# Kernel tuning notes

Measured on AMD Instinct MI355X. Metric: run time of the kernel, lower is better.

## Reference

```python
import jax, jax.numpy as jnp
import numpy as np

B, H, W, DIM = 32, 32, 40, 224
HEADS, DH, WS = 8, 28, 8
INNER = HEADS * DH                      # 224 == DIM (required by spectral branch view)
D_MODEL, D_STATE, D_CONV = 32, 16, 4    # mamba: d_model = H since mode='b h w c'
D_INNER, DT_RANK = 64, 2                # expand=2 -> 64; ceil(32/16)=2
RS = 0.7071067811865476                 # 1/sqrt(2), Haar (db1) filter coefficient


def _ln(x, g, b):
    m = x.mean(-1, keepdims=True)
    v = ((x - m) ** 2).mean(-1, keepdims=True)
    return (x - m) * jax.lax.rsqrt(v + 1e-5) * g + b


def _l2n(x):
    return x / jnp.maximum(jnp.linalg.norm(x, axis=-1, keepdims=True), 1e-12)


def _dwt2(x):
    # Haar level-1 2D DWT, pywt ordering (cA,(cH,cV,cD)); x: [b,c,H,W], even H,W
    lo = (x[..., 0::2] + x[..., 1::2]) * RS
    hi = (x[..., 0::2] - x[..., 1::2]) * RS
    cA = (lo[..., 0::2, :] + lo[..., 1::2, :]) * RS
    cH = (lo[..., 0::2, :] - lo[..., 1::2, :]) * RS
    cV = (hi[..., 0::2, :] + hi[..., 1::2, :]) * RS
    cD = (hi[..., 0::2, :] - hi[..., 1::2, :]) * RS
    return cA, cH, cV, cD


def _iwt2(cA, cH, cV, cD):
    b, c, hh, ww = cA.shape
    lo = jnp.stack([(cA + cH) * RS, (cA - cH) * RS], -2).reshape(b, c, 2 * hh, ww)
    hi = jnp.stack([(cV + cD) * RS, (cV - cD) * RS], -2).reshape(b, c, 2 * hh, ww)
    return jnp.stack([(lo + hi) * RS, (lo - hi) * RS], -1).reshape(b, c, 2 * hh, 2 * ww)


def _mamba(xf, in_proj_W, conv1d_W, conv1d_b, x_proj_W, dt_proj_W, dt_proj_b,
           A_log, Dp, out_proj_W):
    # xf: [b, L, D_MODEL]; mamba_ssm selective-scan math
    bsz = xf.shape[0]
    xz = xf @ in_proj_W                                   # [b,L,2*D_INNER]
    xi, z = xz[..., :D_INNER], xz[..., D_INNER:]
    xc = jax.lax.conv_general_dilated(
        xi.transpose(0, 2, 1), conv1d_W[:, None, :], (1,), [(D_CONV - 1, 0)],
        dimension_numbers=('NCH', 'OIH', 'NCH'), feature_group_count=D_INNER)
    xc = jax.nn.silu(xc + conv1d_b[None, :, None]).transpose(0, 2, 1)  # [b,L,D_INNER]
    x_dbl = xc @ x_proj_W
    dt = jax.nn.softplus(x_dbl[..., :DT_RANK] @ dt_proj_W + dt_proj_b)  # [b,L,D_INNER]
    Bm = x_dbl[..., DT_RANK:DT_RANK + D_STATE]
    Cm = x_dbl[..., DT_RANK + D_STATE:]
    A = -jnp.exp(A_log)                                   # [D_INNER, D_STATE]

    def step(hst, inp):
        dt_t, B_t, C_t, u_t = inp
        dA = jnp.exp(dt_t[:, :, None] * A)                # [b,d,n]
        hst = dA * hst + (dt_t * u_t)[:, :, None] * B_t[:, None, :]
        return hst, jnp.einsum('bdn,bn->bd', hst, C_t)

    h0 = jnp.zeros((bsz, D_INNER, D_STATE), xf.dtype)
    xs = tuple(jnp.moveaxis(t, 1, 0) for t in (dt, Bm, Cm, xc))
    _, ys = jax.lax.scan(step, h0, xs)
    y = jnp.moveaxis(ys, 0, 1) + xc * Dp
    y = y * jax.nn.silu(z)
    return y @ out_proj_W


def setup_inputs():
    key = jax.random.key(0)
    ks = iter(jax.random.split(key, 48))
    def rnd(shape, s=0.02):
        return jax.random.normal(next(ks), shape, jnp.float32) * s
    inp = {}
    inp['x'] = jax.random.normal(next(ks), (B, H, W, DIM), jnp.float32)
    inp['Wq'] = rnd((DIM, INNER)); inp['Wkv'] = rnd((DIM, 2 * INNER))
    inp['ln_g'] = jnp.ones((D_MODEL,)); inp['ln_b'] = jnp.zeros((D_MODEL,))
    inp['in_proj_W'] = rnd((D_MODEL, 2 * D_INNER))
    inp['conv1d_W'] = rnd((D_INNER, D_CONV), 0.3); inp['conv1d_b'] = jnp.zeros((D_INNER,))
    inp['x_proj_W'] = rnd((D_INNER, DT_RANK + 2 * D_STATE), 0.1)
    inp['dt_proj_W'] = rnd((DT_RANK, D_INNER), 0.5)
    inp['dt_proj_b'] = jnp.full((D_INNER,), -4.6, jnp.float32)
    inp['A_log'] = jnp.tile(jnp.log(jnp.arange(1, D_STATE + 1, dtype=jnp.float32))[None], (D_INNER, 1))
    inp['Dp'] = jnp.ones((D_INNER,))
    inp['out_proj_W'] = rnd((D_INNER, D_MODEL))
    inp['skip_scale'] = jnp.ones((1,))
    inp['proj_W'] = rnd((D_MODEL, D_MODEL)); inp['proj_b'] = jnp.zeros((D_MODEL,))
    inp['conv3d_W'] = rnd((1, 1, 5, 5, 5), 0.05); inp['conv3d_b'] = jnp.zeros((1,))
    inp['Wq1'] = rnd((DIM, INNER)); inp['Wkv1'] = rnd((DIM, 2 * INNER))
    inp['pos_emb'] = jnp.clip(rnd((1, HEADS, WS * WS, WS * WS), 1.0), -2.0, 2.0)
    for i in (1, 2, 3, 4):
        inp['Wo%d' % i] = rnd((INNER, DIM)); inp['bo%d' % i] = jnp.zeros((DIM,))
    return inp


def reference(x, Wq, Wkv, ln_g, ln_b, in_proj_W, conv1d_W, conv1d_b, x_proj_W,
              dt_proj_W, dt_proj_b, A_log, Dp, out_proj_W, skip_scale, proj_W,
              proj_b, conv3d_W, conv3d_b, Wq1, Wkv1, pos_emb,
              Wo1, bo1, Wo2, bo2, Wo3, bo3, Wo4, bo4):
    b, h, w, c = x.shape
    scale = DH ** -0.5
    N = h * w
    # ---- spectral branch: channel-wise cosine-similarity attention ----
    x_in = x.reshape(b, N, c)
    q = (x_in @ Wq).reshape(b, N, HEADS, DH).transpose(0, 2, 3, 1)   # [b,Hd,dh,N]
    kv = x_in @ Wkv
    k = kv[..., :INNER].reshape(b, N, HEADS, DH).transpose(0, 2, 3, 1)
    v = kv[..., INNER:].reshape(b, N, HEADS, DH).transpose(0, 2, 3, 1)
    attn = jax.nn.softmax(jnp.einsum('bhin,bhjn->bhij', _l2n(k), _l2n(q)) * scale, -1)
    xa = jnp.einsum('bhij,bhjn->bhin', attn, v)                      # [b,Hd,dh,N]
    x = xa.transpose(0, 3, 1, 2).reshape(b, h, w, c) + x
    # ---- MambaLayer (mode 'b h w c': channel axis = h) + residual ----
    xf = x.reshape(b, h, w * c).transpose(0, 2, 1)                   # [b, w*c, h]
    xn = _ln(xf, ln_g, ln_b)
    xm = _mamba(xn, in_proj_W, conv1d_W, conv1d_b, x_proj_W, dt_proj_W,
                dt_proj_b, A_log, Dp, out_proj_W) + skip_scale * xn
    xm = _ln(xm, ln_g, ln_b) @ proj_W + proj_b
    x = xm.transpose(0, 2, 1).reshape(b, h, w, c) + x
    # ---- Conv3d 5x5x5 fusion over (h,w,c) ----
    x = jax.lax.conv_general_dilated(x[:, None], conv3d_W, (1, 1, 1), [(2, 2)] * 3,
            dimension_numbers=('NCDHW', 'OIDHW', 'NCDHW'))[:, 0] + conv3d_b[0]
    # ---- local branch: Haar subbands + windowed attention with pos bias ----
    cA, cH, cV, cD = _dwt2(x.transpose(0, 3, 1, 2))
    ha, wa = cA.shape[2], cA.shape[3]
    pad_h, pad_w = (-ha) % WS, (-wa) % WS

    def win_attn(sub, Wo, bo):
        s = jnp.pad(sub, ((0, 0), (0, 0), (0, pad_h), (0, pad_w)), mode='reflect')
        Hs, Ws_ = s.shape[2], s.shape[3]
        xw = s.reshape(b, c, Hs // WS, WS, Ws_ // WS, WS).transpose(0, 2, 4, 3, 5, 1)
        xw = xw.reshape(-1, WS * WS, c)
        qw = (xw @ Wq1).reshape(-1, WS * WS, HEADS, DH).transpose(0, 2, 1, 3) * scale
        kvw = xw @ Wkv1
        kw = kvw[..., :INNER].reshape(-1, WS * WS, HEADS, DH).transpose(0, 2, 1, 3)
        vw = kvw[..., INNER:].reshape(-1, WS * WS, HEADS, DH).transpose(0, 2, 1, 3)
        a = jax.nn.softmax(jnp.einsum('bhid,bhjd->bhij', qw, kw) + pos_emb, -1)
        o = jnp.einsum('bhij,bhjd->bhid', a, vw).transpose(0, 2, 1, 3).reshape(-1, WS * WS, INNER)
        o = (o @ Wo + bo).reshape(b, Hs // WS, Ws_ // WS, WS, WS, c).transpose(0, 1, 3, 2, 4, 5)
        return o.reshape(b, Hs, Ws_, c)[:, :ha, :wa, :].transpose(0, 3, 1, 2)

    out = _iwt2(win_attn(cA, Wo1, bo1), win_attn(cH, Wo2, bo2),
                win_attn(cV, Wo3, bo3), win_attn(cD, Wo4, bo4))
    return out.transpose(0, 2, 3, 1)
```

## Files before the change

kernel.cpp:

```cpp
#include <hip/hip_runtime.h>
#include <hip/hip_bf16.h>
#include <math.h>

typedef __hip_bfloat16 bf16;
typedef __attribute__((ext_vector_type(8))) short bf16x8;
typedef __attribute__((ext_vector_type(4))) float f32x4;

__device__ __forceinline__ float b2f(bf16 v){ return __bfloat162float(v); }
__device__ __forceinline__ bf16  f2b(float v){ return __float2bfloat16(v); }
__device__ __forceinline__ float bfbits(unsigned u){ return __uint_as_float(u << 16); }
__device__ __forceinline__ unsigned short b2us(bf16 v){ union { bf16 b; unsigned short u; } c; c.b = v; return c.u; }
__device__ __forceinline__ void unpack8(uint4 q, float* f){
  f[0]=bfbits(q.x&0xffffu); f[1]=bfbits(q.x>>16);
  f[2]=bfbits(q.y&0xffffu); f[3]=bfbits(q.y>>16);
  f[4]=bfbits(q.z&0xffffu); f[5]=bfbits(q.z>>16);
  f[6]=bfbits(q.w&0xffffu); f[7]=bfbits(q.w>>16);
}
__device__ __forceinline__ uint4 pack8f(const float* f){
  uint4 q;
  q.x = (unsigned)b2us(f2b(f[0])) | ((unsigned)b2us(f2b(f[1]))<<16);
  q.y = (unsigned)b2us(f2b(f[2])) | ((unsigned)b2us(f2b(f[3]))<<16);
  q.z = (unsigned)b2us(f2b(f[4])) | ((unsigned)b2us(f2b(f[5]))<<16);
  q.w = (unsigned)b2us(f2b(f[6])) | ((unsigned)b2us(f2b(f[7]))<<16);
  return q;
}

#define NTOK 1280
#define LSEQ 8960
#define CHLEN 140
#define ATT_SCALE 0.1889822365046136f
#define LOG2E 1.4426950408889634f

__global__ __launch_bounds__(256) void cvt_bf16_kernel(const float* __restrict__ src, bf16* __restrict__ dst, int n8) {
  int i = blockIdx.x*256 + threadIdx.x;
  if (i >= n8) return;
  const float4* s = (const float4*)(src + (size_t)i*8);
  float4 a = s[0], b = s[1];
  float f[8] = {a.x,a.y,a.z,a.w,b.x,b.y,b.z,b.w};
  *(uint4*)(dst + (size_t)i*8) = pack8f(f);
}

__global__ __launch_bounds__(256) void transpose_bf16_kernel(const float* __restrict__ W, bf16* __restrict__ Wt,
                                                             int K, int N) {
  int idx = blockIdx.x*256 + threadIdx.x;
  if (idx >= N*K) return;
  int n = idx / K, k = idx % K;
  Wt[idx] = f2b(W[(size_t)k*N + n]);
}

__global__ __launch_bounds__(256) void mfma_gemm_kernel(const bf16* __restrict__ A, const bf16* __restrict__ Bt,
                                                        float* __restrict__ C, int M, int N, int K) {
  __shared__ short As[64][40];
  __shared__ short Bs[64][40];
  const int tid = threadIdx.x;
  const int wave = tid >> 6, lane = tid & 63;
  const int m0 = blockIdx.y*64, n0 = blockIdx.x*64;
  const int lrow = tid >> 2, lseg = (tid & 3) * 8;
  const int mrow = wave*16 + (lane & 15);
  const int kq = (lane >> 4) * 8;
  f32x4 acc[4] = {};
  for (int k0 = 0; k0 < K; k0 += 32) {
    uint4 av = *(const uint4*)(A + (size_t)(m0+lrow)*K + k0 + lseg);
    uint4 bv = make_uint4(0u,0u,0u,0u);
    if (n0 + lrow < N) bv = *(const uint4*)(Bt + (size_t)(n0+lrow)*K + k0 + lseg);
    __syncthreads();
    *(uint4*)&As[lrow][lseg] = av;
    *(uint4*)&Bs[lrow][lseg] = bv;
    __syncthreads();
    bf16x8 af = *(const bf16x8*)&As[mrow][kq];
#pragma unroll
    for (int nt = 0; nt < 4; ++nt) {
      bf16x8 bfv = *(const bf16x8*)&Bs[nt*16 + (lane & 15)][kq];
      acc[nt] = __builtin_amdgcn_mfma_f32_16x16x32_bf16(af, bfv, acc[nt], 0, 0, 0);
    }
  }
  const int quad = lane >> 4, col = lane & 15;
#pragma unroll
  for (int nt = 0; nt < 4; ++nt) {
    int n = n0 + nt*16 + col;
    if (n >= N) continue;
#pragma unroll
    for (int r = 0; r < 4; ++r) {
      int m = m0 + wave*16 + quad*4 + r;
      C[(size_t)m*N + n] = acc[nt][r];
    }
  }
}

__global__ __launch_bounds__(256) void zero_kernel(float* __restrict__ p, int n) {
  int i = blockIdx.x*256 + threadIdx.x;
  if (i < n) p[i] = 0.f;
}

__global__ __launch_bounds__(256) void colnorm_kernel(const float* __restrict__ qb, const float* __restrict__ kvb,
                                                      float* __restrict__ nqs, float* __restrict__ nks) {
  const int b  = blockIdx.x >> 4;
  const int nc = blockIdx.x & 15;
  const int tid = threadIdx.x;
  __shared__ float lq[224], lk[224];
  if (tid < 224) { lq[tid] = 0.f; lk[tid] = 0.f; }
  __syncthreads();
  const int n0 = nc * 80;
  for (int idx = tid; idx < 80*224; idx += 256) {
    int n = n0 + idx / 224, c = idx % 224;
    float v = qb[((size_t)(b*NTOK + n))*224 + c];
    atomicAdd(&lq[c], v*v);
    float w = kvb[((size_t)(b*NTOK + n))*448 + c];
    atomicAdd(&lk[c], w*w);
  }
  __syncthreads();
  if (tid < 224) {
    atomicAdd(&nqs[b*224 + tid], lq[tid]);
    atomicAdd(&nks[b*224 + tid], lk[tid]);
  }
}

__global__ __launch_bounds__(256) void gram_kernel(const float* __restrict__ qb, const float* __restrict__ kvb,
                                                   const float* __restrict__ nqs, const float* __restrict__ nks,
                                                   float* __restrict__ attnA) {
  const int b = blockIdx.x >> 3, hd = blockIdx.x & 7;
  const int tid = threadIdx.x;
  __shared__ float kt[32][28];
  __shared__ float qt[32][28];
  __shared__ float sc[784];
  float acc[4] = {0.f,0.f,0.f,0.f};
  for (int nt = 0; nt < NTOK; nt += 32) {
    __syncthreads();
    for (int idx = tid; idx < 896; idx += 256) {
      int r = idx / 28, c = idx % 28;
      kt[r][c] = kvb[((size_t)(b*NTOK + nt + r))*448 + hd*28 + c];
      qt[r][c] = qb [((size_t)(b*NTOK + nt + r))*224 + hd*28 + c];
    }
    __syncthreads();
#pragma unroll
    for (int p = 0; p < 4; ++p) {
      int idx = tid + p*256;
      if (idx < 784) {
        int i = idx / 28, j = idx % 28;
        float s = 0.f;
#pragma unroll
        for (int r = 0; r < 32; ++r) s = fmaf(kt[r][i], qt[r][j], s);
        acc[p] += s;
      }
    }
  }
  __syncthreads();
#pragma unroll
  for (int p = 0; p < 4; ++p) {
    int idx = tid + p*256;
    if (idx < 784) {
      int i = idx / 28, j = idx % 28;
      float nk = fmaxf(sqrtf(nks[b*224 + hd*28 + i]), 1e-12f);
      float nq = fmaxf(sqrtf(nqs[b*224 + hd*28 + j]), 1e-12f);
      sc[idx] = acc[p] * ATT_SCALE / (nk * nq);
    }
  }
  __syncthreads();
  if (tid < 28) {
    int i = tid;
    float mx = -1e30f;
#pragma unroll
    for (int j = 0; j < 28; ++j) mx = fmaxf(mx, sc[i*28+j]);
    float e[28]; float s = 0.f;
#pragma unroll
    for (int j = 0; j < 28; ++j) { e[j] = expf(sc[i*28+j] - mx); s += e[j]; }
    float inv = 1.f / s;
#pragma unroll
    for (int j = 0; j < 28; ++j) attnA[(size_t)blockIdx.x*784 + i*28 + j] = e[j]*inv;
  }
}

__global__ __launch_bounds__(256) void applyattn_kernel(const float* __restrict__ attnA, const float* __restrict__ kvb,
                                                        const float* __restrict__ x, float* __restrict__ x1) {
  const int bhd = blockIdx.x;
  const int b = bhd >> 3, hd = bhd & 7;
  const int tid = threadIdx.x;
  __shared__ float a[784];
  for (int idx = tid; idx < 784; idx += 256) a[idx] = attnA[(size_t)bhd*784 + idx];
  __syncthreads();
  const int i = tid % 28;
  const int n = blockIdx.y * 9 + tid / 28;
  if (tid < 252 && n < NTOK) {
    const float* vrow = &kvb[((size_t)(b*NTOK + n))*448 + 224 + hd*28];
    float s = 0.f;
#pragma unroll
    for (int j = 0; j < 28; ++j) s = fmaf(a[i*28+j], vrow[j], s);
    size_t o = ((size_t)(b*NTOK + n))*224 + hd*28 + i;
    x1[o] = s + x[o];
  }
}

__global__ __launch_bounds__(256) void mamba_in_kernel(const float* __restrict__ x1, const float* __restrict__ lng,
                                                       const float* __restrict__ lnb, const float* __restrict__ Wip,
                                                       bf16* __restrict__ xi) {
  __shared__ float W[2048];
  __shared__ float g[32], bb[32];
  const int tid = threadIdx.x;
  const int b = blockIdx.y;
  const int t = blockIdx.x*256 + tid;
  for (int idx = tid; idx < 2048; idx += 256) {
    int d = idx >> 5, m = idx & 31;
    W[idx] = Wip[m*128 + d];
  }
  if (tid < 32) { g[tid] = lng[tid]; bb[tid] = lnb[tid]; }
  __syncthreads();
  float xv[32];
  float mean = 0.f;
#pragma unroll
  for (int m = 0; m < 32; ++m) { xv[m] = x1[((size_t)(b*32+m))*LSEQ + t]; mean += xv[m]; }
  mean *= (1.f/32.f);
  float var = 0.f;
#pragma unroll
  for (int m = 0; m < 32; ++m) { float d = xv[m]-mean; var = fmaf(d, d, var); }
  var *= (1.f/32.f);
  const float rstd = rsqrtf(var + 1e-5f);
  float xn[32];
#pragma unroll
  for (int m = 0; m < 32; ++m) xn[m] = (xv[m]-mean)*rstd*g[m] + bb[m];
  bf16* row = xi + ((size_t)b*LSEQ + t)*64;
#pragma unroll
  for (int gi = 0; gi < 8; ++gi) {
    float sv[8];
#pragma unroll
    for (int j = 0; j < 8; ++j) {
      int d = gi*8 + j;
      float s = 0.f;
#pragma unroll
      for (int mq = 0; mq < 8; ++mq) {
        float4 w = *(const float4*)&W[d*32 + mq*4];
        s = fmaf(xn[mq*4+0], w.x, s);
        s = fmaf(xn[mq*4+1], w.y, s);
        s = fmaf(xn[mq*4+2], w.z, s);
        s = fmaf(xn[mq*4+3], w.w, s);
      }
      sv[j] = s;
    }
    *(uint4*)(row + gi*8) = pack8f(sv);
  }
}

__global__ __launch_bounds__(256) void mamba_conv_kernel(const bf16* __restrict__ xi, const float* __restrict__ convW,
    const float* __restrict__ convB, const float* __restrict__ xpW, const float* __restrict__ dtW,
    const float* __restrict__ dtB, bf16* __restrict__ xc, bf16* __restrict__ dts,
    bf16* __restrict__ Bc, bf16* __restrict__ Ccs) {
  __shared__ float xit[67][65];
  __shared__ float xct[64][65];
  __shared__ float xdbl[64][36];
  __shared__ float Wc[256], bcs[64], Wxp[2176], Wdt[128], bdt[64];
  const int tid = threadIdx.x;
  const int b = blockIdx.y;
  const int t0 = blockIdx.x * 64;

  if (tid < 256) Wc[tid] = convW[tid];
  for (int idx = tid; idx < 2176; idx += 256) Wxp[idx] = xpW[idx];
  if (tid < 128) Wdt[tid] = dtW[tid];
  if (tid < 64) { bcs[tid] = convB[tid]; bdt[tid] = dtB[tid]; }
  for (int idx = tid; idx < 67*8; idx += 256) {
    const int row = idx >> 3, seg = idx & 7;
    const int gt = t0 + row - 3;
    float f[8];
    if (gt >= 0) {
      uint4 q = *(const uint4*)(xi + ((size_t)b*LSEQ + gt)*64 + seg*8);
      unpack8(q, f);
    } else {
#pragma unroll
      for (int j = 0; j < 8; ++j) f[j] = 0.f;
    }
#pragma unroll
    for (int j = 0; j < 8; ++j) xit[row][seg*8 + j] = f[j];
  }
  __syncthreads();

  {
    const int tl = tid >> 2, cg = tid & 3;
    float sv[16];
#pragma unroll
    for (int j = 0; j < 16; ++j) {
      const int d = cg*16 + j;
      float s = bcs[d];
      s = fmaf(xit[tl+0][d], Wc[d*4+0], s);
      s = fmaf(xit[tl+1][d], Wc[d*4+1], s);
      s = fmaf(xit[tl+2][d], Wc[d*4+2], s);
      s = fmaf(xit[tl+3][d], Wc[d*4+3], s);
      s = s / (1.f + expf(-s));
      xct[tl][d] = s;
      sv[j] = s;
    }
    bf16* out = xc + ((size_t)b*LSEQ + t0 + tl)*64 + cg*16;
    *(uint4*)(out)     = pack8f(sv);
    *(uint4*)(out + 8) = pack8f(sv + 8);
  }
  __syncthreads();

  {
    const int tl = tid & 63, g = tid >> 6;
    for (int n = g; n < 34; n += 4) {
      float s = 0.f;
#pragma unroll
      for (int d = 0; d < 64; ++d) s = fmaf(xct[tl][d], Wxp[d*34 + n], s);
      xdbl[tl][n] = s;
    }
  }
  __syncthreads();

  if (tid < 256) {
    const int which = tid >> 7;
    const int idx = tid & 127;
    const int tl = idx >> 1, half = idx & 1;
    const float* src = &xdbl[tl][2 + which*16 + half*8];
    bf16* dst = (which ? Ccs : Bc) + ((size_t)b*LSEQ + t0 + tl)*16 + half*8;
    *(uint4*)dst = pack8f(src);
  }
  {
    const int tl = tid >> 2, cg = tid & 3;
    const float x0 = xdbl[tl][0], x1v = xdbl[tl][1];
    float sv[16];
#pragma unroll
    for (int j = 0; j < 16; ++j) {
      const int d = cg*16 + j;
      float v = fmaf(x0, Wdt[d], fmaf(x1v, Wdt[64+d], bdt[d]));
      v = (v > 20.f) ? v : log1pf(expf(v));
      sv[j] = v;
    }
    bf16* out = dts + ((size_t)b*LSEQ + t0 + tl)*64 + cg*16;
    *(uint4*)(out)     = pack8f(sv);
    *(uint4*)(out + 8) = pack8f(sv + 8);
  }
}

__global__ __launch_bounds__(256) void scan1_kernel(const bf16* __restrict__ dts, const bf16* __restrict__ xc,
    const bf16* __restrict__ Bc, const float* __restrict__ Alog, float* __restrict__ P, float* __restrict__ F) {
  const int b = blockIdx.x >> 6, chk = blockIdx.x & 63;
  const int tid = threadIdx.x;
  const int d = tid >> 2, ng = tid & 3;
  float A2[4], Pr[4], Fr[4];
#pragma unroll
  for (int j = 0; j < 4; ++j) {
    A2[j] = -expf(Alog[d*16 + ng*4 + j]) * LOG2E;
    Pr[j] = 1.f; Fr[j] = 0.f;
  }
  const size_t tbase = (size_t)b*LSEQ + (size_t)chk*CHLEN;
  for (int i = 0; i < CHLEN; ++i) {
    const size_t t = tbase + i;
    float dtv = b2f(dts[t*64 + d]);
    float u   = b2f(xc [t*64 + d]);
    float du  = dtv*u;
    uint2 bq = *(const uint2*)(Bc + t*16 + ng*4);
    float Bv[4];
    Bv[0]=bfbits(bq.x&0xffffu); Bv[1]=bfbits(bq.x>>16);
    Bv[2]=bfbits(bq.y&0xffffu); Bv[3]=bfbits(bq.y>>16);
#pragma unroll
    for (int j = 0; j < 4; ++j) {
      float a = exp2f(dtv*A2[j]);
      Pr[j] *= a;
      Fr[j] = fmaf(a, Fr[j], du*Bv[j]);
    }
  }
  const size_t o = (((size_t)(b*64 + chk))*64 + d)*16 + ng*4;
  *(float4*)(P + o) = make_float4(Pr[0],Pr[1],Pr[2],Pr[3]);
  *(float4*)(F + o) = make_float4(Fr[0],Fr[1],Fr[2],Fr[3]);
}

__global__ __launch_bounds__(256) void scan2_kernel(const float* __restrict__ P, const float* __restrict__ F,
                                                    float* __restrict__ H0) {
  const int idx = blockIdx.x*256 + threadIdx.x;
  const int b = idx >> 10, dn = idx & 1023;
  const size_t base = (size_t)b*64*1024 + dn;
  float h = 0.f;
  for (int ch = 0; ch < 64; ++ch) {
    const size_t a = base + (size_t)ch*1024;
    H0[a] = h;
    h = fmaf(P[a], h, F[a]);
  }
}

__global__ __launch_bounds__(256) void scan3_kernel(const bf16* __restrict__ dts, const bf16* __restrict__ xc,
    const bf16* __restrict__ Bc, const bf16* __restrict__ Ccs, const float* __restrict__ Alog,
    const float* __restrict__ Dp, const float* __restrict__ H0, bf16* __restrict__ y) {
  const int b = blockIdx.x >> 6, chk = blockIdx.x & 63;
  const int tid = threadIdx.x;
  const int d = tid >> 2, ng = tid & 3;
  float A2[4], h[4];
  const size_t hb = (((size_t)(b*64 + chk))*64 + d)*16 + ng*4;
  float4 h0 = *(const float4*)(H0 + hb);
  h[0]=h0.x; h[1]=h0.y; h[2]=h0.z; h[3]=h0.w;
#pragma unroll
  for (int j = 0; j < 4; ++j) A2[j] = -expf(Alog[d*16 + ng*4 + j]) * LOG2E;
  const float Dpd = Dp[d];
  const size_t tbase = (size_t)b*LSEQ + (size_t)chk*CHLEN;
  for (int i = 0; i < CHLEN; ++i) {
    const size_t t = tbase + i;
    float dtv = b2f(dts[t*64 + d]);
    float u   = b2f(xc [t*64 + d]);
    float du  = dtv*u;
    uint2 bq = *(const uint2*)(Bc  + t*16 + ng*4);
    uint2 cq = *(const uint2*)(Ccs + t*16 + ng*4);
    float Bv[4], Cv[4];
    Bv[0]=bfbits(bq.x&0xffffu); Bv[1]=bfbits(bq.x>>16);
    Bv[2]=bfbits(bq.y&0xffffu); Bv[3]=bfbits(bq.y>>16);
    Cv[0]=bfbits(cq.x&0xffffu); Cv[1]=bfbits(cq.x>>16);
    Cv[2]=bfbits(cq.y&0xffffu); Cv[3]=bfbits(cq.y>>16);
    float p = 0.f;
#pragma unroll
    for (int j = 0; j < 4; ++j) {
      float a = exp2f(dtv*A2[j]);
      h[j] = fmaf(a, h[j], du*Bv[j]);
      p = fmaf(h[j], Cv[j], p);
    }
    p += __shfl_xor(p, 1);
    p += __shfl_xor(p, 2);
    if (ng == 0) y[t*64 + d] = f2b(p + u*Dpd);
  }
}

__global__ __launch_bounds__(256) void mamba_out_kernel(float* __restrict__ x1, const bf16* __restrict__ y,
    const float* __restrict__ lng, const float* __restrict__ lnb, const float* __restrict__ Wip,
    const float* __restrict__ Wout, const float* __restrict__ skipp, const float* __restrict__ Wp,
    const float* __restrict__ pbias) {
  __shared__ float Wzt[2048];
  __shared__ float Wo[2048];
  __shared__ float Pwt[1024];
  __shared__ float g[32], bb[32], pb[32];
  __shared__ float sskip;
  const int tid = threadIdx.x;
  for (int idx = tid; idx < 2048; idx += 256) {
    int d = idx >> 5, m = idx & 31;
    Wzt[idx] = Wip[m*128 + 64 + d];
  }
  for (int idx = tid; idx < 2048; idx += 256) Wo[idx] = Wout[idx];
  for (int idx = tid; idx < 1024; idx += 256) {
    int m2 = idx >> 5, m = idx & 31;
    Pwt[idx] = Wp[m*32 + m2];
  }
  if (tid < 32) { g[tid] = lng[tid]; bb[tid] = lnb[tid]; pb[tid] = pbias[tid]; }
  if (tid == 0) sskip = skipp[0];
  __syncthreads();
  const int b = blockIdx.y;
  const int t = blockIdx.x*256 + tid;
  float xv[32];
  float mean = 0.f;
#pragma unroll
  for (int m = 0; m < 32; ++m) { xv[m] = x1[((size_t)(b*32+m))*LSEQ + t]; mean += xv[m]; }
  mean *= (1.f/32.f);
  float var = 0.f;
#pragma unroll
  for (int m = 0; m < 32; ++m) { float d = xv[m]-mean; var = fmaf(d, d, var); }
  var *= (1.f/32.f);
  const float rstd = rsqrtf(var + 1e-5f);
  float xn[32];
#pragma unroll
  for (int m = 0; m < 32; ++m) xn[m] = (xv[m]-mean)*rstd*g[m] + bb[m];
  float out[32] = {};
  const bf16* yrow = y + ((size_t)b*LSEQ + t)*64;
#pragma unroll
  for (int gi = 0; gi < 8; ++gi) {
    uint4 q = *(const uint4*)(yrow + gi*8);
    float yv8[8]; unpack8(q, yv8);
#pragma unroll
    for (int j = 0; j < 8; ++j) {
      int d = gi*8 + j;
      float zd = 0.f;
#pragma unroll
      for (int mq = 0; mq < 8; ++mq) {
        float4 w = *(const float4*)&Wzt[d*32 + mq*4];
        zd = fmaf(xn[mq*4+0], w.x, zd);
        zd = fmaf(xn[mq*4+1], w.y, zd);
        zd = fmaf(xn[mq*4+2], w.z, zd);
        zd = fmaf(xn[mq*4+3], w.w, zd);
      }
      float gd = yv8[j] * zd / (1.f + expf(-zd));
#pragma unroll
      for (int mq = 0; mq < 8; ++mq) {
        float4 w = *(const float4*)&Wo[d*32 + mq*4];
        out[mq*4+0] = fmaf(gd, w.x, out[mq*4+0]);
        out[mq*4+1] = fmaf(gd, w.y, out[mq*4+1]);
        out[mq*4+2] = fmaf(gd, w.z, out[mq*4+2]);
        out[mq*4+3] = fmaf(gd, w.w, out[mq*4+3]);
      }
    }
  }
#pragma unroll
  for (int m = 0; m < 32; ++m) out[m] = fmaf(sskip, xn[m], out[m]);
  float mean2 = 0.f;
#pragma unroll
  for (int m = 0; m < 32; ++m) mean2 += out[m];
  mean2 *= (1.f/32.f);
  float var2 = 0.f;
#pragma unroll
  for (int m = 0; m < 32; ++m) { float d = out[m]-mean2; var2 = fmaf(d, d, var2); }
  var2 *= (1.f/32.f);
  const float rstd2 = rsqrtf(var2 + 1e-5f);
#pragma unroll
  for (int m = 0; m < 32; ++m) out[m] = (out[m]-mean2)*rstd2*g[m] + bb[m];
  for (int m2 = 0; m2 < 32; ++m2) {
    float r = pb[m2];
#pragma unroll
    for (int mq = 0; mq < 8; ++mq) {
      float4 w = *(const float4*)&Pwt[m2*32 + mq*4];
      r = fmaf(out[mq*4+0], w.x, r);
      r = fmaf(out[mq*4+1], w.y, r);
      r = fmaf(out[mq*4+2], w.z, r);
      r = fmaf(out[mq*4+3], w.w, r);
    }
    x1[((size_t)(b*32+m2))*LSEQ + t] = r + xv[m2];
  }
}

__global__ __launch_bounds__(256) void conv3d_kernel(const float* __restrict__ x2, const float* __restrict__ w,
                                                     const float* __restrict__ bias, float* __restrict__ x3) {
  __shared__ float ww[125];
  __shared__ float b0;
  const int tid = threadIdx.x;
  if (tid < 125) ww[tid] = w[tid];
  if (tid == 0) b0 = bias[0];
  __syncthreads();
  const int gid = blockIdx.x*256 + tid;
  const int kg = gid % 28;
  int r = gid / 28;
  const int j = r % 40; r /= 40;
  const int i = r % 32; const int b = r / 32;
  const int k0 = kg * 8;
  float acc[8] = {};
  for (int di = 0; di < 5; ++di) {
    int ii = i + di - 2; if (ii < 0 || ii >= 32) continue;
    for (int dj = 0; dj < 5; ++dj) {
      int jj = j + dj - 2; if (jj < 0 || jj >= 40) continue;
      const float* row = &x2[(((size_t)(b*32+ii))*40 + jj)*224];
      float f[16];
#pragma unroll
      for (int off = 0; off < 4; ++off) {
        int base = k0 + off*4 - 4;
        if (base >= 0 && base <= 220) {
          float4 v = *(const float4*)(row + base);
          f[off*4+0]=v.x; f[off*4+1]=v.y; f[off*4+2]=v.z; f[off*4+3]=v.w;
        } else {
          f[off*4+0]=0.f; f[off*4+1]=0.f; f[off*4+2]=0.f; f[off*4+3]=0.f;
        }
      }
      const float* wr = &ww[(di*5+dj)*5];
#pragma unroll
      for (int dk = 0; dk < 5; ++dk) {
        float wv = wr[dk];
#pragma unroll
        for (int o = 0; o < 8; ++o) acc[o] = fmaf(wv, f[o+dk+2], acc[o]);
      }
    }
  }
  float* out = x3 + (size_t)gid*8;
  *(float4*)(out)     = make_float4(acc[0]+b0, acc[1]+b0, acc[2]+b0, acc[3]+b0);
  *(float4*)(out + 4) = make_float4(acc[4]+b0, acc[5]+b0, acc[6]+b0, acc[7]+b0);
}

__global__ __launch_bounds__(256) void dwtwin_kernel(const float* __restrict__ x3, bf16* __restrict__ xw) {
  const int gid = blockIdx.x*256 + threadIdx.x;
  const int ch = gid % 224; int r = gid / 224;
  const int tok = r % 64; const int win = r / 64;
  const int b = win / 6, rr = win % 6, wy = rr / 3, wx = rr % 3;
  const int ty = tok >> 3, tx = tok & 7;
  const int i = wy*8 + ty;
  const int jp = wx*8 + tx;
  const int j = (jp < 20) ? jp : (38 - jp);
  const size_t base = (((size_t)(b*32 + 2*i))*40 + 2*j)*224 + ch;
  const float v00 = x3[base];
  const float v01 = x3[base + 224];
  const float v10 = x3[base + 8960];
  const float v11 = x3[base + 8960 + 224];
  const size_t o = (size_t)r*224 + ch;
  const size_t SW = 2752512;
  xw[o]        = f2b(0.5f*(v00 + v01 + v10 + v11));
  xw[SW + o]   = f2b(0.5f*(v00 + v01 - v10 - v11));
  xw[2*SW + o] = f2b(0.5f*(v00 - v01 + v10 - v11));
  xw[3*SW + o] = f2b(0.5f*(v00 - v01 - v10 + v11));
}

__global__ __launch_bounds__(256) void winattn_kernel(const float* __restrict__ qw, const float* __restrict__ kvw,
                                                      const float* __restrict__ pos, bf16* __restrict__ ow) {
  const int win = blockIdx.x >> 3, hd = blockIdx.x & 7;
  const int tid = threadIdx.x;
  __shared__ float qs[1792], ks[1792], vs[1792];
  __shared__ float sc[4096];
  for (int idx = tid; idx < 1792; idx += 256) {
    int tok = idx / 28, d = idx % 28;
    qs[idx] = qw [((size_t)(win*64+tok))*224 + hd*28 + d] * ATT_SCALE;
    ks[idx] = kvw[((size_t)(win*64+tok))*448 + hd*28 + d];
    vs[idx] = kvw[((size_t)(win*64+tok))*448 + 224 + hd*28 + d];
  }
  __syncthreads();
#pragma unroll
  for (int p = 0; p < 16; ++p) {
    int idx = tid + p*256;
    int i = idx >> 6, j = idx & 63;
    float a = 0.f;
#pragma unroll
    for (int d = 0; d < 28; ++d) a = fmaf(qs[i*28+d], ks[j*28+d], a);
    sc[idx] = a + pos[(hd*64 + i)*64 + j];
  }
  __syncthreads();
  if (tid < 64) {
    const int i = tid;
    float mx = -1e30f;
#pragma unroll
    for (int j = 0; j < 64; ++j) mx = fmaxf(mx, sc[i*64+j]);
    float s = 0.f;
#pragma unroll
    for (int j = 0; j < 64; ++j) { float e = expf(sc[i*64+j] - mx); sc[i*64+j] = e; s += e; }
    const float inv = 1.f / s;
#pragma unroll
    for (int j = 0; j < 64; ++j) sc[i*64+j] *= inv;
  }
  __syncthreads();
  for (int idx = tid; idx < 1792; idx += 256) {
    int i = idx / 28, d = idx % 28;
    float a = 0.f;
#pragma unroll
    for (int j = 0; j < 64; ++j) a = fmaf(sc[i*64+j], vs[j*28+d], a);
    ow[((size_t)(win*64+i))*224 + hd*28 + d] = f2b(a);
  }
}

__global__ __launch_bounds__(256) void scatter_kernel(const float* __restrict__ proj, const float* __restrict__ bo,
                                                      float* __restrict__ wa) {
  const int gid = blockIdx.x*256 + threadIdx.x;
  const int ch = gid % 224; int r = gid / 224;
  const int tok = r % 64; const int win = r / 64;
  const int b = win / 6, rr = win % 6, wy = rr / 3, wx = rr % 3;
  const int ty = tok >> 3, tx = tok & 7;
  const int i = wy*8 + ty;
  const int jp = wx*8 + tx;
  if (jp < 20)
    wa[(((size_t)(b*16+i))*20 + jp)*224 + ch] = proj[gid] + bo[ch];
}

__global__ __launch_bounds__(256) void iwt_kernel(const float* __restrict__ wa, float* __restrict__ out) {
  const int gid = blockIdx.x*256 + threadIdx.x;
  const int ch = gid % 224; int r = gid / 224;
  const int j2 = r % 40; r /= 40;
  const int i2 = r % 32; const int b = r / 32;
  const size_t SB = 2293760;
  const size_t base = (((size_t)(b*16 + (i2>>1)))*20 + (j2>>1))*224 + ch;
  const float cA = wa[base];
  const float cH = wa[SB + base];
  const float cV = wa[2*SB + base];
  const float cD = wa[3*SB + base];
  const float sp = (i2 & 1) ? -1.f : 1.f;
  const float sq = (j2 & 1) ? -1.f : 1.f;
  out[gid] = 0.5f*(cA + sp*cH + sq*cV + sp*sq*cD);
}

extern "C" void kernel_launch(void* const* d_in, const int* in_sizes, int n_in,
                              void* d_out, int out_size, void* d_ws, size_t ws_size,
                              hipStream_t stream) {
  (void)in_sizes; (void)n_in; (void)out_size; (void)ws_size;
  const float* x     = (const float*)d_in[0];
  const float* Wq    = (const float*)d_in[1];
  const float* Wkv   = (const float*)d_in[2];
  const float* lng   = (const float*)d_in[3];
  const float* lnb   = (const float*)d_in[4];
  const float* Wip   = (const float*)d_in[5];
  const float* convW = (const float*)d_in[6];
  const float* convB = (const float*)d_in[7];
  const float* xpW   = (const float*)d_in[8];
  const float* dtW   = (const float*)d_in[9];
  const float* dtB   = (const float*)d_in[10];
  const float* Alog  = (const float*)d_in[11];
  const float* Dp    = (const float*)d_in[12];
  const float* Wout  = (const float*)d_in[13];
  const float* skip  = (const float*)d_in[14];
  const float* Wp    = (const float*)d_in[15];
  const float* pbias = (const float*)d_in[16];
  const float* c3w   = (const float*)d_in[17];
  const float* c3b   = (const float*)d_in[18];
  const float* Wq1   = (const float*)d_in[19];
  const float* Wkv1  = (const float*)d_in[20];
  const float* pos   = (const float*)d_in[21];

  char* ws = (char*)d_ws;
  float* x1    = (float*)(ws + 0);
  float* qbuf  = (float*)(ws + 36700160);
  float* kvbuf = (float*)(ws + 73400320);
  bf16*  WqT   = (bf16*) (ws + 146800640);
  bf16*  WkvT  = (bf16*) (ws + 146900992);
  bf16*  xbf   = (bf16*) (ws + 147101696);
  bf16*  xi    = (bf16*) (ws + 36700160);
  bf16*  xc    = (bf16*) (ws + 73400320);
  bf16*  dts   = (bf16*) (ws + 110100480);
  bf16*  Bcb   = (bf16*) (ws + 146800640);
  bf16*  Ccb   = (bf16*) (ws + 155975680);
  float* Pbuf  = (float*)(ws + 165150720);
  float* Fbuf  = (float*)(ws + 173539328);
  float* H0    = (float*)(ws + 181927936);
  bf16*  ybuf  = (bf16*) (ws + 36700160);
  float* x3    = (float*)(ws + 36700160);
  bf16*  xw    = (bf16*) (ws + 73400320);
  float* qw    = (float*)(ws + 95420416);
  float* kvw   = (float*)(ws + 106430464);
  bf16*  owb   = (bf16*) (ws + 128450560);
  bf16*  Wq1T  = (bf16*) (ws + 134000640);
  bf16*  Wkv1T = (bf16*) (ws + 134100992);
  bf16*  WoT0  = (bf16*) (ws + 134301696);
  bf16*  WoT1  = (bf16*) (ws + 134402048);
  bf16*  WoT2  = (bf16*) (ws + 134502400);
  bf16*  WoT3  = (bf16*) (ws + 134602752);
  float* projt = qw;
  float* wab   = (float*)(ws + 0);
  float* nqs   = (float*)(ws + 190316544);
  float* nks   = (float*)(ws + 190345216);
  float* attnA = (float*)(ws + 190373888);
  bf16* WoTs[4] = {WoT0, WoT1, WoT2, WoT3};

  zero_kernel<<<56, 256, 0, stream>>>(nqs, 14336);
  cvt_bf16_kernel<<<4480, 256, 0, stream>>>(x, xbf, 1146880);
  transpose_bf16_kernel<<<196, 256, 0, stream>>>(Wq,  WqT,  224, 224);
  transpose_bf16_kernel<<<392, 256, 0, stream>>>(Wkv, WkvT, 224, 448);
  mfma_gemm_kernel<<<dim3(4,640), 256, 0, stream>>>(xbf, WqT,  qbuf,  40960, 224, 224);
  mfma_gemm_kernel<<<dim3(7,640), 256, 0, stream>>>(xbf, WkvT, kvbuf, 40960, 448, 224);
  colnorm_kernel<<<512, 256, 0, stream>>>(qbuf, kvbuf, nqs, nks);
  gram_kernel<<<256, 256, 0, stream>>>(qbuf, kvbuf, nqs, nks, attnA);
  applyattn_kernel<<<dim3(256,143), 256, 0, stream>>>(attnA, kvbuf, x, x1);

  mamba_in_kernel<<<dim3(35,32), 256, 0, stream>>>(x1, lng, lnb, Wip, xi);
  mamba_conv_kernel<<<dim3(140,32), 256, 0, stream>>>(xi, convW, convB, xpW, dtW, dtB, xc, dts, Bcb, Ccb);
  scan1_kernel<<<2048, 256, 0, stream>>>(dts, xc, Bcb, Alog, Pbuf, Fbuf);
  scan2_kernel<<<128, 256, 0, stream>>>(Pbuf, Fbuf, H0);
  scan3_kernel<<<2048, 256, 0, stream>>>(dts, xc, Bcb, Ccb, Alog, Dp, H0, ybuf);
  mamba_out_kernel<<<dim3(35,32), 256, 0, stream>>>(x1, ybuf, lng, lnb, Wip, Wout, skip, Wp, pbias);

  conv3d_kernel<<<4480, 256, 0, stream>>>(x1, c3w, c3b, x3);

  dwtwin_kernel<<<10752, 256, 0, stream>>>(x3, xw);
  transpose_bf16_kernel<<<196, 256, 0, stream>>>(Wq1,  Wq1T,  224, 224);
  transpose_bf16_kernel<<<392, 256, 0, stream>>>(Wkv1, Wkv1T, 224, 448);
  for (int s = 0; s < 4; ++s)
    transpose_bf16_kernel<<<196, 256, 0, stream>>>((const float*)d_in[22 + 2*s], WoTs[s], 224, 224);
  for (int s = 0; s < 4; ++s) {
    const float* bo = (const float*)d_in[23 + 2*s];
    const bf16* xws = xw + (size_t)s * 2752512;
    mfma_gemm_kernel<<<dim3(4,192), 256, 0, stream>>>(xws, Wq1T,  qw,  12288, 224, 224);
    mfma_gemm_kernel<<<dim3(7,192), 256, 0, stream>>>(xws, Wkv1T, kvw, 12288, 448, 224);
    winattn_kernel<<<1536, 256, 0, stream>>>(qw, kvw, pos, owb);
    mfma_gemm_kernel<<<dim3(4,192), 256, 0, stream>>>(owb, WoTs[s], projt, 12288, 224, 224);
    scatter_kernel<<<10752, 256, 0, stream>>>(projt, bo, wab + (size_t)s * 2293760);
  }
  iwt_kernel<<<35840, 256, 0, stream>>>(wab, (float*)d_out);
}
```

Measured before the change: 1.694 ms.

## Keep mamba conv and x_proj in registers with shuffle reductions

The mamba_conv kernel no longer stages the input window, conv output and x_proj results in shared-memory tiles. Each thread now loads its four causal input rows straight into registers and computes its 16 conv channels there. It then produces partial x_proj dot products that are reduced across the four channel-group lanes with xor shuffles. A small new kernel pre-transposes x_proj_W so the per-output weight reads are contiguous float4 loads. This removes two block barriers and a large amount of shared memory, in exchange for more registers per thread, redundant shuffle work and an extra tiny launch whose buffer reuses the nqs workspace region.

```diff
diff --git a/kernel.cpp b/kernel.cpp
--- a/kernel.cpp
+++ b/kernel.cpp
@@ -46,6 +46,13 @@
   if (idx >= N*K) return;
   int n = idx / K, k = idx % K;
   Wt[idx] = f2b(W[(size_t)k*N + n]);
+}
+
+__global__ __launch_bounds__(256) void transpose_xp_kernel(const float* __restrict__ W, float* __restrict__ Wt) {
+  int idx = blockIdx.x*256 + threadIdx.x;
+  if (idx >= 2176) return;
+  int n = idx >> 6, d = idx & 63;
+  Wt[idx] = W[d*34 + n];
 }
 
 __global__ __launch_bounds__(256) void mfma_gemm_kernel(const bf16* __restrict__ A, const bf16* __restrict__ Bt,
@@ -240,91 +247,99 @@
 }
 
 __global__ __launch_bounds__(256) void mamba_conv_kernel(const bf16* __restrict__ xi, const float* __restrict__ convW,
-    const float* __restrict__ convB, const float* __restrict__ xpW, const float* __restrict__ dtW,
+    const float* __restrict__ convB, const float* __restrict__ xpWT, const float* __restrict__ dtW,
     const float* __restrict__ dtB, bf16* __restrict__ xc, bf16* __restrict__ dts,
     bf16* __restrict__ Bc, bf16* __restrict__ Ccs) {
-  __shared__ float xit[67][65];
-  __shared__ float xct[64][65];
-  __shared__ float xdbl[64][36];
-  __shared__ float Wc[256], bcs[64], Wxp[2176], Wdt[128], bdt[64];
+  __shared__ float Wc[256], bcs[64], Wxpt[2176], Wdt[128], bdt[64];
   const int tid = threadIdx.x;
   const int b = blockIdx.y;
   const int t0 = blockIdx.x * 64;
+  const int tl = tid >> 2, cg = tid & 3;
 
   if (tid < 256) Wc[tid] = convW[tid];
-  for (int idx = tid; idx < 2176; idx += 256) Wxp[idx] = xpW[idx];
+  for (int idx = tid; idx < 2176; idx += 256) Wxpt[idx] = xpWT[idx];
   if (tid < 128) Wdt[tid] = dtW[tid];
   if (tid < 64) { bcs[tid] = convB[tid]; bdt[tid] = dtB[tid]; }
-  for (int idx = tid; idx < 67*8; idx += 256) {
-    const int row = idx >> 3, seg = idx & 7;
-    const int gt = t0 + row - 3;
-    float f[8];
+  __syncthreads();
+
+  const int t = t0 + tl;
+  uint4 r4[4][2];
+#pragma unroll
+  for (int k = 0; k < 4; ++k) {
+    const int gt = t - 3 + k;
     if (gt >= 0) {
-      uint4 q = *(const uint4*)(xi + ((size_t)b*LSEQ + gt)*64 + seg*8);
-      unpack8(q, f);
+      const bf16* rp = xi + ((size_t)b*LSEQ + gt)*64 + cg*16;
+      r4[k][0] = *(const uint4*)(rp);
+      r4[k][1] = *(const uint4*)(rp + 8);
     } else {
-#pragma unroll
-      for (int j = 0; j < 8; ++j) f[j] = 0.f;
-    }
-#pragma unroll
-    for (int j = 0; j < 8; ++j) xit[row][seg*8 + j] = f[j];
-  }
-  __syncthreads();
-
+      r4[k][0] = make_uint4(0u,0u,0u,0u);
+      r4[k][1] = make_uint4(0u,0u,0u,0u);
+    }
+  }
+
+  float sv[16];
+#pragma unroll
+  for (int j = 0; j < 16; ++j) {
+    const int d = cg*16 + j;
+    float4 wc = *(const float4*)&Wc[d*4];
+    float s = bcs[d];
+#pragma unroll
+    for (int k = 0; k < 4; ++k) {
+      const uint4 q = r4[k][j >> 3];
+      const int w = (j >> 1) & 3;
+      unsigned comp = (w==0) ? q.x : (w==1) ? q.y : (w==2) ? q.z : q.w;
+      float xv = bfbits((j & 1) ? (comp >> 16) : (comp & 0xffffu));
+      float wk = (k==0) ? wc.x : (k==1) ? wc.y : (k==2) ? wc.z : wc.w;
+      s = fmaf(xv, wk, s);
+    }
+    s = s / (1.f + expf(-s));
+    sv[j] = s;
+  }
   {
-    const int tl = tid >> 2, cg = tid & 3;
-    float sv[16];
+    bf16* out = xc + ((size_t)b*LSEQ + t)*64 + cg*16;
+    *(uint4*)(out)     = pack8f(sv);
+    *(uint4*)(out + 8) = pack8f(sv + 8);
+  }
+
+  float xdb[34];
+#pragma unroll
+  for (int n = 0; n < 34; ++n) {
+    float s = 0.f;
+#pragma unroll
+    for (int dq = 0; dq < 4; ++dq) {
+      float4 w = *(const float4*)&Wxpt[n*64 + cg*16 + dq*4];
+      s = fmaf(sv[dq*4+0], w.x, s);
+      s = fmaf(sv[dq*4+1], w.y, s);
+      s = fmaf(sv[dq*4+2], w.z, s);
+      s = fmaf(sv[dq*4+3], w.w, s);
+    }
+    s += __shfl_xor(s, 1);
+    s += __shfl_xor(s, 2);
+    xdb[n] = s;
+  }
+
+  {
+    float svdt[16];
 #pragma unroll
     for (int j = 0; j < 16; ++j) {
       const int d = cg*16 + j;
-      float s = bcs[d];
-      s = fmaf(xit[tl+0][d], Wc[d*4+0], s);
-      s = fmaf(xit[tl+1][d], Wc[d*4+1], s);
-      s = fmaf(xit[tl+2][d], Wc[d*4+2], s);
-      s = fmaf(xit[tl+3][d], Wc[d*4+3], s);
-      s = s / (1.f + expf(-s));
-      xct[tl][d] = s;
-      sv[j] = s;
-    }
-    bf16* out = xc + ((size_t)b*LSEQ + t0 + tl)*64 + cg*16;
-    *(uint4*)(out)     = pack8f(sv);
-    *(uint4*)(out + 8) = pack8f(sv + 8);
-  }
-  __syncthreads();
-
-  {
-    const int tl = tid & 63, g = tid >> 6;
-    for (int n = g; n < 34; n += 4) {
-      float s = 0.f;
-#pragma unroll
-      for (int d = 0; d < 64; ++d) s = fmaf(xct[tl][d], Wxp[d*34 + n], s);
-      xdbl[tl][n] = s;
-    }
-  }
-  __syncthreads();
-
-  if (tid < 256) {
-    const int which = tid >> 7;
-    const int idx = tid & 127;
-    const int tl = idx >> 1, half = idx & 1;
-    const float* src = &xdbl[tl][2 + which*16 + half*8];
-    bf16* dst = (which ? Ccs : Bc) + ((size_t)b*LSEQ + t0 + tl)*16 + half*8;
-    *(uint4*)dst = pack8f(src);
-  }
-  {
-    const int tl = tid >> 2, cg = tid & 3;
-    const float x0 = xdbl[tl][0], x1v = xdbl[tl][1];
-    float sv[16];
-#pragma unroll
-    for (int j = 0; j < 16; ++j) {
-      const int d = cg*16 + j;
-      float v = fmaf(x0, Wdt[d], fmaf(x1v, Wdt[64+d], bdt[d]));
+      float v = fmaf(xdb[0], Wdt[d], fmaf(xdb[1], Wdt[64+d], bdt[d]));
       v = (v > 20.f) ? v : log1pf(expf(v));
-      sv[j] = v;
-    }
-    bf16* out = dts + ((size_t)b*LSEQ + t0 + tl)*64 + cg*16;
-    *(uint4*)(out)     = pack8f(sv);
-    *(uint4*)(out + 8) = pack8f(sv + 8);
+      svdt[j] = v;
+    }
+    bf16* out = dts + ((size_t)b*LSEQ + t)*64 + cg*16;
+    *(uint4*)(out)     = pack8f(svdt);
+    *(uint4*)(out + 8) = pack8f(svdt + 8);
+  }
+
+  if (cg == 0) {
+    bf16* dst = Bc + ((size_t)b*LSEQ + t)*16;
+    *(uint4*)(dst)     = pack8f(&xdb[2]);
+    *(uint4*)(dst + 8) = pack8f(&xdb[10]);
+  } else if (cg == 1) {
+    bf16* dst = Ccs + ((size_t)b*LSEQ + t)*16;
+    *(uint4*)(dst)     = pack8f(&xdb[18]);
+    *(uint4*)(dst + 8) = pack8f(&xdb[26]);
   }
 }
 
@@ -706,6 +721,7 @@
   float* nqs   = (float*)(ws + 190316544);
   float* nks   = (float*)(ws + 190345216);
   float* attnA = (float*)(ws + 190373888);
+  float* WxpT  = (float*)(ws + 190316544);
   bf16* WoTs[4] = {WoT0, WoT1, WoT2, WoT3};
 
   zero_kernel<<<56, 256, 0, stream>>>(nqs, 14336);
@@ -716,10 +732,11 @@
   mfma_gemm_kernel<<<dim3(7,640), 256, 0, stream>>>(xbf, WkvT, kvbuf, 40960, 448, 224);
   colnorm_kernel<<<512, 256, 0, stream>>>(qbuf, kvbuf, nqs, nks);
   gram_kernel<<<256, 256, 0, stream>>>(qbuf, kvbuf, nqs, nks, attnA);
+  transpose_xp_kernel<<<9, 256, 0, stream>>>(xpW, WxpT);
   applyattn_kernel<<<dim3(256,143), 256, 0, stream>>>(attnA, kvbuf, x, x1);
 
   mamba_in_kernel<<<dim3(35,32), 256, 0, stream>>>(x1, lng, lnb, Wip, xi);
-  mamba_conv_kernel<<<dim3(140,32), 256, 0, stream>>>(xi, convW, convB, xpW, dtW, dtB, xc, dts, Bcb, Ccb);
+  mamba_conv_kernel<<<dim3(140,32), 256, 0, stream>>>(xi, convW, convB, WxpT, dtW, dtB, xc, dts, Bcb, Ccb);
   scan1_kernel<<<2048, 256, 0, stream>>>(dts, xc, Bcb, Alog, Pbuf, Fbuf);
   scan2_kernel<<<128, 256, 0, stream>>>(Pbuf, Fbuf, H0);
   scan3_kernel<<<2048, 256, 0, stream>>>(dts, xc, Bcb, Ccb, Alog, Dp, H0, ybuf);
```

After: 1.656 ms. 1.02x faster.
